# Performance work log

Hardware: AMD Instinct MI355X
Metric: run time of the kernel (lower is better)

Reference implementation:

```python
import jax, jax.numpy as jnp
import numpy as np

B, T, IN, H, L, OUT = 32, 512, 256, 1024, 2, 256


def setup_inputs() -> dict:
    key = jax.random.key(0)
    ks = jax.random.split(key, 12)
    s_in = 1.0 / np.sqrt(H)
    inp = {
        "input": jax.random.normal(ks[0], (B, T, IN), dtype=jnp.float32),
        # layer 0 GRU params (PyTorch layout: [3H, in], gate order r,z,n)
        "w_ih0": jax.random.uniform(ks[1], (3 * H, IN), jnp.float32, -s_in, s_in),
        "w_hh0": jax.random.uniform(ks[2], (3 * H, H), jnp.float32, -s_in, s_in),
        "b_ih0": jax.random.uniform(ks[3], (3 * H,), jnp.float32, -s_in, s_in),
        "b_hh0": jax.random.uniform(ks[4], (3 * H,), jnp.float32, -s_in, s_in),
        # layer 1 GRU params
        "w_ih1": jax.random.uniform(ks[5], (3 * H, H), jnp.float32, -s_in, s_in),
        "w_hh1": jax.random.uniform(ks[6], (3 * H, H), jnp.float32, -s_in, s_in),
        "b_ih1": jax.random.uniform(ks[7], (3 * H,), jnp.float32, -s_in, s_in),
        "b_hh1": jax.random.uniform(ks[8], (3 * H,), jnp.float32, -s_in, s_in),
        # final linear
        "fc_w": jax.random.uniform(ks[9], (OUT, H), jnp.float32, -s_in, s_in),
        "fc_b": jax.random.uniform(ks[10], (OUT,), jnp.float32, -s_in, s_in),
    }
    return inp


def _gru_layer(x, h0, w_ih, w_hh, b_ih, b_hh):
    # x: [B, T, D]; h0: [B, H]. Precompute all input projections at once.
    gx = jnp.einsum("btd,gd->btg", x, w_ih) + b_ih  # [B, T, 3H]

    def step(h, gx_t):
        gh = h @ w_hh.T + b_hh  # [B, 3H]
        xr, xz, xn = jnp.split(gx_t, 3, axis=-1)
        hr, hz, hn = jnp.split(gh, 3, axis=-1)
        r = jax.nn.sigmoid(xr + hr)
        z = jax.nn.sigmoid(xz + hz)
        n = jnp.tanh(xn + r * hn)
        h_new = (1.0 - z) * n + z * h
        return h_new, h_new

    h_last, hs = jax.lax.scan(step, h0, jnp.swapaxes(gx, 0, 1))  # hs: [T, B, H]
    return jnp.swapaxes(hs, 0, 1), h_last


def reference(input, w_ih0, w_hh0, b_ih0, b_hh0, w_ih1, w_hh1, b_ih1, b_hh1, fc_w, fc_b):
    b = input.shape[0]
    h0 = jnp.zeros((b, H), dtype=input.dtype)
    out0, h_last0 = _gru_layer(input, h0, w_ih0, w_hh0, b_ih0, b_hh0)
    out1, h_last1 = _gru_layer(out0, h0, w_ih1, w_hh1, b_ih1, b_hh1)
    h_n = jnp.stack([h_last0, h_last1], axis=0)  # [L, B, H]
    logits = out1[:, -1, :] @ fc_w.T + fc_b  # [B, OUT]
    return jax.nn.sigmoid(logits), h_n
```

## Files before the change

kernel.cpp:

```cpp
#include <hip/hip_runtime.h>

#define BB 32
#define TT 512
#define INW 256
#define HH 1024
#define OUTW 256
#define SLOT 32768

typedef __attribute__((ext_vector_type(8))) short short8;
typedef __attribute__((ext_vector_type(4))) float floatx4;

#define RSWZ(i) ((i) ^ ((((i) >> 5) & 3) << 2))

__device__ __forceinline__ unsigned short f2bf(float f) {
    unsigned int u = __float_as_uint(f);
    u = (u + 0x7fffu + ((u >> 16) & 1u)) >> 16;
    return (unsigned short)u;
}
__device__ __forceinline__ float bf2f(unsigned short h) {
    return __uint_as_float(((unsigned int)h) << 16);
}
__device__ __forceinline__ float fast_tanh(float x) {
    return 2.f / (1.f + __expf(-2.f * x)) - 1.f;
}

__global__ void cast_f32_bf16(const float* __restrict__ src,
                              unsigned short* __restrict__ dst, int n) {
    int i = blockIdx.x * blockDim.x + threadIdx.x;
    int stride = gridDim.x * blockDim.x;
    for (; i < n; i += stride) dst[i] = f2bf(src[i]);
}

template <int K>
__global__ __launch_bounds__(256) void gemm_gx(const unsigned short* __restrict__ X,
                                               const unsigned short* __restrict__ W,
                                               const float* __restrict__ bias,
                                               unsigned short* __restrict__ Cout) {
    __shared__ __align__(16) unsigned short As[64 * 40];
    __shared__ __align__(16) unsigned short Bs[64 * 40];
    int bid = blockIdx.x;
    int tn = bid % 48, tm = bid / 48;
    int tid = threadIdx.x;
    int lane = tid & 63, wv = tid >> 6;
    int wm = wv >> 1, wn = wv & 1;
    int l15 = lane & 15, q = lane >> 4;
    floatx4 acc[2][2] = {};
    int r = tid >> 2, kq = (tid & 3) * 8;
    const unsigned short* xrow = X + (size_t)(tm * 64 + r) * K;
    const unsigned short* wrow = W + (size_t)(tn * 64 + r) * K;
    const int NK = K / 32;
    for (int kk = 0; kk < NK; ++kk) {
        int k0 = kk * 32;
        *(short8*)&As[r * 40 + kq] = *(const short8*)&xrow[k0 + kq];
        *(short8*)&Bs[r * 40 + kq] = *(const short8*)&wrow[k0 + kq];
        __syncthreads();
        short8 a0 = *(const short8*)&As[(wm * 32 + l15) * 40 + q * 8];
        short8 a1 = *(const short8*)&As[(wm * 32 + 16 + l15) * 40 + q * 8];
        short8 b0 = *(const short8*)&Bs[(wn * 32 + l15) * 40 + q * 8];
        short8 b1 = *(const short8*)&Bs[(wn * 32 + 16 + l15) * 40 + q * 8];
        acc[0][0] = __builtin_amdgcn_mfma_f32_16x16x32_bf16(a0, b0, acc[0][0], 0, 0, 0);
        acc[0][1] = __builtin_amdgcn_mfma_f32_16x16x32_bf16(a0, b1, acc[0][1], 0, 0, 0);
        acc[1][0] = __builtin_amdgcn_mfma_f32_16x16x32_bf16(a1, b0, acc[1][0], 0, 0, 0);
        acc[1][1] = __builtin_amdgcn_mfma_f32_16x16x32_bf16(a1, b1, acc[1][1], 0, 0, 0);
        __syncthreads();
    }
    for (int mi = 0; mi < 2; ++mi)
        for (int ni = 0; ni < 2; ++ni) {
            int col = tn * 64 + wn * 32 + ni * 16 + l15;
            float bv = bias[col];
            int row0 = tm * 64 + wm * 32 + mi * 16 + q * 4;
            for (int rr = 0; rr < 4; ++rr) {
                Cout[(size_t)(row0 + rr) * 3072 + col] = f2bf(acc[mi][ni][rr] + bv);
            }
        }
}

__global__ __launch_bounds__(512, 2) void gru_fused(
    const unsigned short* __restrict__ gx0, const unsigned short* __restrict__ whh0,
    const float* __restrict__ bhh0, const unsigned short* __restrict__ wih1,
    const unsigned short* __restrict__ whh1, const float* __restrict__ bih1,
    const float* __restrict__ bhh1, unsigned short* __restrict__ ring0,
    unsigned short* __restrict__ ring1, float* __restrict__ hn0,
    float* __restrict__ hn1, unsigned int* __restrict__ flags) {
    __shared__ __align__(16) float red[8 * 6 * 64 * 4];
    const int bid = blockIdx.x;
    const int tid = threadIdx.x;
    const int lane = tid & 63, wv = tid >> 6;
    const int l15 = lane & 15, q = lane >> 4;
    const int gb = tid >> 3, gjh = tid & 7;
    const int gmi = gb >> 4, greg = gb & 3;
    const int grl = ((gb & 15) >> 2) * 16 + 2 * gjh;

    if (bid < 64) {
        const int j0 = bid * 16;
        const int kbase = wv * 128;
        const unsigned int* fl0 = flags + ((bid & 7) << 8);
        short8 Wr[4], Wz[4], Wn[4];
        {
            const unsigned short* wr0 = whh0 + (size_t)(j0 + l15) * HH;
            const unsigned short* wr1 = whh0 + (size_t)(1024 + j0 + l15) * HH;
            const unsigned short* wr2 = whh0 + (size_t)(2048 + j0 + l15) * HH;
#pragma unroll
            for (int s = 0; s < 4; ++s) {
                int k = kbase + s * 32 + q * 8;
                Wr[s] = *(const short8*)&wr0[k];
                Wz[s] = *(const short8*)&wr1[k];
                Wn[s] = *(const short8*)&wr2[k];
            }
        }
        float bR[2], bZ[2], bN[2], hpriv[2] = {0.f, 0.f};
        unsigned int pxr = 0, pxz = 0, pxn = 0;
        const unsigned short* gxp = nullptr;
        if (tid < 256) {
            int jj = j0 + 2 * gjh;
#pragma unroll
            for (int i = 0; i < 2; ++i) {
                bR[i] = bhh0[jj + i];
                bZ[i] = bhh0[1024 + jj + i];
                bN[i] = bhh0[2048 + jj + i];
            }
            gxp = gx0 + (size_t)gb * TT * 3072 + jj;
            pxr = *(const unsigned int*)(gxp);
            pxz = *(const unsigned int*)(gxp + 1024);
            pxn = *(const unsigned int*)(gxp + 2048);
        }

        for (int t = 0; t < TT; ++t) {
            if (t > 0 && wv == 0) {
                unsigned int target = (unsigned int)t;
                while (true) {
                    unsigned int v = __hip_atomic_load(fl0 + lane, __ATOMIC_RELAXED,
                                                       __HIP_MEMORY_SCOPE_AGENT);
                    if (__all((int)(v >= target))) break;
                    __builtin_amdgcn_s_sleep(1);
                }
            }
            __syncthreads();
            const unsigned short* hc = ring0 + (size_t)t * SLOT;
            unsigned int cxr = pxr, cxz = pxz, cxn = pxn;

            short8 A0[4], A1[4];
#pragma unroll
            for (int s = 0; s < 4; ++s) {
                int k = kbase + s * 32 + q * 8;
                int cb = (k >> 4) << 9, ko = k & 15;
                A0[s] = *(const short8*)&hc[cb + (l15 << 4) + ko];
                A1[s] = *(const short8*)&hc[cb + ((16 + l15) << 4) + ko];
            }
            floatx4 acc[6] = {};
#pragma unroll
            for (int s = 0; s < 4; ++s) {
                acc[0] = __builtin_amdgcn_mfma_f32_16x16x32_bf16(A0[s], Wr[s], acc[0], 0, 0, 0);
                acc[1] = __builtin_amdgcn_mfma_f32_16x16x32_bf16(A0[s], Wz[s], acc[1], 0, 0, 0);
                acc[2] = __builtin_amdgcn_mfma_f32_16x16x32_bf16(A0[s], Wn[s], acc[2], 0, 0, 0);
                acc[3] = __builtin_amdgcn_mfma_f32_16x16x32_bf16(A1[s], Wr[s], acc[3], 0, 0, 0);
                acc[4] = __builtin_amdgcn_mfma_f32_16x16x32_bf16(A1[s], Wz[s], acc[4], 0, 0, 0);
                acc[5] = __builtin_amdgcn_mfma_f32_16x16x32_bf16(A1[s], Wn[s], acc[5], 0, 0, 0);
            }
#pragma unroll
            for (int tl = 0; tl < 6; ++tl)
                *(floatx4*)&red[RSWZ(((wv * 6 + tl) * 64 + lane) * 4)] = acc[tl];
            __syncthreads();

            float hnew[2];
            if (tid < 256) {
#pragma unroll
                for (int i = 0; i < 2; ++i) {
                    int rl = grl + i;
                    float gr = 0.f, gz = 0.f, gn = 0.f;
#pragma unroll
                    for (int w = 0; w < 8; ++w) {
                        gr += red[RSWZ(((w * 6 + gmi * 3 + 0) * 64 + rl) * 4 + greg)];
                        gz += red[RSWZ(((w * 6 + gmi * 3 + 1) * 64 + rl) * 4 + greg)];
                        gn += red[RSWZ(((w * 6 + gmi * 3 + 2) * 64 + rl) * 4 + greg)];
                    }
                    float xr = bf2f((unsigned short)(i ? (cxr >> 16) : (cxr & 0xffffu)));
                    float xz = bf2f((unsigned short)(i ? (cxz >> 16) : (cxz & 0xffffu)));
                    float xn = bf2f((unsigned short)(i ? (cxn >> 16) : (cxn & 0xffffu)));
                    float rg = 1.f / (1.f + __expf(-(xr + gr + bR[i])));
                    float zg = 1.f / (1.f + __expf(-(xz + gz + bZ[i])));
                    float ng = fast_tanh(xn + rg * (gn + bN[i]));
                    hnew[i] = (1.f - zg) * ng + zg * hpriv[i];
                    hpriv[i] = hnew[i];
                }
                unsigned int hpack =
                    (unsigned int)f2bf(hnew[0]) | ((unsigned int)f2bf(hnew[1]) << 16);
                unsigned int* dst =
                    (unsigned int*)(ring0 + (size_t)(t + 1) * SLOT) + (bid << 8) + tid;
                __hip_atomic_store(dst, hpack, __ATOMIC_RELAXED,
                                   __HIP_MEMORY_SCOPE_AGENT);
                asm volatile("s_waitcnt vmcnt(0)" ::: "memory");
            }
            __syncthreads();
            if (tid < 8)
                __hip_atomic_store(flags + (tid << 8) + bid, (unsigned int)(t + 1),
                                   __ATOMIC_RELAXED, __HIP_MEMORY_SCOPE_AGENT);
            if (tid < 256) {
                if (t == TT - 1) {
                    hn0[gb * HH + j0 + 2 * gjh] = hnew[0];
                    hn0[gb * HH + j0 + 2 * gjh + 1] = hnew[1];
                }
                if (t + 1 < TT) {
                    const unsigned short* g2 = gxp + (size_t)(t + 1) * 3072;
                    pxr = *(const unsigned int*)(g2);
                    pxz = *(const unsigned int*)(g2 + 1024);
                    pxn = *(const unsigned int*)(g2 + 2048);
                }
            }
        }
    } else {
        const int b2 = bid - 64;
        const int j0 = b2 * 16;
        const bool isx = (wv >= 4);
        const int kbase = (wv & 3) * 256;
        const unsigned int* fl1 = flags + 2048 + ((b2 & 7) << 8);
        const unsigned int* fl0 = flags + ((b2 & 7) << 8);
        short8 Wr[8], Wz[8], Wn[8];
        {
            const unsigned short* wsrc = isx ? wih1 : whh1;
            const unsigned short* w0 = wsrc + (size_t)(j0 + l15) * HH;
            const unsigned short* w1 = wsrc + (size_t)(1024 + j0 + l15) * HH;
            const unsigned short* w2 = wsrc + (size_t)(2048 + j0 + l15) * HH;
#pragma unroll
            for (int s = 0; s < 8; ++s) {
                int k = kbase + s * 32 + q * 8;
                Wr[s] = *(const short8*)&w0[k];
                Wz[s] = *(const short8*)&w1[k];
                Wn[s] = *(const short8*)&w2[k];
            }
        }
        float cR[2], cZ[2], cNx[2], cNh[2], hpriv[2] = {0.f, 0.f};
        if (tid < 256) {
            int jj = j0 + 2 * gjh;
#pragma unroll
            for (int i = 0; i < 2; ++i) {
                cR[i] = bih1[jj + i] + bhh1[jj + i];
                cZ[i] = bih1[1024 + jj + i] + bhh1[1024 + jj + i];
                cNx[i] = bih1[2048 + jj + i];
                cNh[i] = bhh1[2048 + jj + i];
            }
        }

        for (int t = 0; t < TT; ++t) {
            if (t > 0 && wv == 0) {
                unsigned int target = (unsigned int)t;
                while (true) {
                    unsigned int v = __hip_atomic_load(fl1 + lane, __ATOMIC_RELAXED,
                                                       __HIP_MEMORY_SCOPE_AGENT);
                    if (__all((int)(v >= target))) break;
                    __builtin_amdgcn_s_sleep(1);
                }
            }
            if (wv == 4) {
                unsigned int target = (unsigned int)(t + 1);
                while (true) {
                    unsigned int v = __hip_atomic_load(fl0 + lane, __ATOMIC_RELAXED,
                                                       __HIP_MEMORY_SCOPE_AGENT);
                    if (__all((int)(v >= target))) break;
                    __builtin_amdgcn_s_sleep(1);
                }
            }
            __syncthreads();
            const unsigned short* src =
                isx ? (ring0 + (size_t)(t + 1) * SLOT) : (ring1 + (size_t)t * SLOT);

            short8 A0[8], A1[8];
#pragma unroll
            for (int s = 0; s < 8; ++s) {
                int k = kbase + s * 32 + q * 8;
                int cb = (k >> 4) << 9, ko = k & 15;
                A0[s] = *(const short8*)&src[cb + (l15 << 4) + ko];
                A1[s] = *(const short8*)&src[cb + ((16 + l15) << 4) + ko];
            }
            floatx4 acc[6] = {};
#pragma unroll
            for (int s = 0; s < 8; ++s) {
                acc[0] = __builtin_amdgcn_mfma_f32_16x16x32_bf16(A0[s], Wr[s], acc[0], 0, 0, 0);
                acc[1] = __builtin_amdgcn_mfma_f32_16x16x32_bf16(A0[s], Wz[s], acc[1], 0, 0, 0);
                acc[2] = __builtin_amdgcn_mfma_f32_16x16x32_bf16(A0[s], Wn[s], acc[2], 0, 0, 0);
                acc[3] = __builtin_amdgcn_mfma_f32_16x16x32_bf16(A1[s], Wr[s], acc[3], 0, 0, 0);
                acc[4] = __builtin_amdgcn_mfma_f32_16x16x32_bf16(A1[s], Wz[s], acc[4], 0, 0, 0);
                acc[5] = __builtin_amdgcn_mfma_f32_16x16x32_bf16(A1[s], Wn[s], acc[5], 0, 0, 0);
            }
#pragma unroll
            for (int tl = 0; tl < 6; ++tl)
                *(floatx4*)&red[RSWZ(((wv * 6 + tl) * 64 + lane) * 4)] = acc[tl];
            __syncthreads();

            float hnew[2];
            if (tid < 256) {
#pragma unroll
                for (int i = 0; i < 2; ++i) {
                    int rl = grl + i;
                    float gr = 0.f, gz = 0.f, hn = 0.f, xn = 0.f;
#pragma unroll
                    for (int w = 0; w < 4; ++w) {
                        gr += red[RSWZ(((w * 6 + gmi * 3 + 0) * 64 + rl) * 4 + greg)];
                        gz += red[RSWZ(((w * 6 + gmi * 3 + 1) * 64 + rl) * 4 + greg)];
                        hn += red[RSWZ(((w * 6 + gmi * 3 + 2) * 64 + rl) * 4 + greg)];
                    }
#pragma unroll
                    for (int w = 4; w < 8; ++w) {
                        gr += red[RSWZ(((w * 6 + gmi * 3 + 0) * 64 + rl) * 4 + greg)];
                        gz += red[RSWZ(((w * 6 + gmi * 3 + 1) * 64 + rl) * 4 + greg)];
                        xn += red[RSWZ(((w * 6 + gmi * 3 + 2) * 64 + rl) * 4 + greg)];
                    }
                    float rg = 1.f / (1.f + __expf(-(gr + cR[i])));
                    float zg = 1.f / (1.f + __expf(-(gz + cZ[i])));
                    float ng = fast_tanh(xn + cNx[i] + rg * (hn + cNh[i]));
                    hnew[i] = (1.f - zg) * ng + zg * hpriv[i];
                    hpriv[i] = hnew[i];
                }
                unsigned int hpack =
                    (unsigned int)f2bf(hnew[0]) | ((unsigned int)f2bf(hnew[1]) << 16);
                unsigned int* dst =
                    (unsigned int*)(ring1 + (size_t)(t + 1) * SLOT) + (b2 << 8) + tid;
                __hip_atomic_store(dst, hpack, __ATOMIC_RELAXED,
                                   __HIP_MEMORY_SCOPE_AGENT);
                asm volatile("s_waitcnt vmcnt(0)" ::: "memory");
            }
            __syncthreads();
            if (tid < 8)
                __hip_atomic_store(flags + 2048 + (tid << 8) + b2, (unsigned int)(t + 1),
                                   __ATOMIC_RELAXED, __HIP_MEMORY_SCOPE_AGENT);
            if (tid < 256 && t == TT - 1) {
                hn1[gb * HH + j0 + 2 * gjh] = hnew[0];
                hn1[gb * HH + j0 + 2 * gjh + 1] = hnew[1];
            }
        }
    }
}

__global__ void fc_out(const unsigned short* __restrict__ h1bf,
                       const float* __restrict__ fcw, const float* __restrict__ fcb,
                       float* __restrict__ out) {
    int b = blockIdx.x, o = threadIdx.x;
    const float* wr = fcw + (size_t)o * HH;
    float acc = fcb[o];
    for (int k = 0; k < HH; k += 16) {
        const unsigned short* hp = h1bf + ((k >> 4) << 9) + (b << 4);
#pragma unroll
        for (int i = 0; i < 16; ++i) acc += bf2f(hp[i]) * wr[k + i];
    }
    out[b * OUTW + o] = 1.f / (1.f + expf(-acc));
}

extern "C" void kernel_launch(void* const* d_in, const int* in_sizes, int n_in,
                              void* d_out, int out_size, void* d_ws, size_t ws_size,
                              hipStream_t stream) {
    (void)in_sizes; (void)n_in; (void)out_size; (void)ws_size;
    const float* input = (const float*)d_in[0];
    const float* w_ih0 = (const float*)d_in[1];
    const float* w_hh0 = (const float*)d_in[2];
    const float* b_ih0 = (const float*)d_in[3];
    const float* b_hh0 = (const float*)d_in[4];
    const float* w_ih1 = (const float*)d_in[5];
    const float* w_hh1 = (const float*)d_in[6];
    const float* b_ih1 = (const float*)d_in[7];
    const float* b_hh1 = (const float*)d_in[8];
    const float* fc_w = (const float*)d_in[9];
    const float* fc_b = (const float*)d_in[10];
    float* out = (float*)d_out;

    char* ws = (char*)d_ws;
    size_t off = 0;
    auto alloc = [&](size_t bytes) {
        void* p = ws + off;
        off += (bytes + 255) & ~(size_t)255;
        return p;
    };
    unsigned int* flags = (unsigned int*)alloc(16384);
    unsigned short* ring0 = (unsigned short*)alloc((size_t)(TT + 1) * SLOT * 2);
    unsigned short* ring1 = (unsigned short*)alloc((size_t)(TT + 1) * SLOT * 2);
    unsigned short* gx0 = (unsigned short*)alloc((size_t)16384 * 3072 * 2);
    unsigned short* in_bf = (unsigned short*)alloc((size_t)16384 * 256 * 2);
    unsigned short* wih0_bf = (unsigned short*)alloc((size_t)3072 * 256 * 2);
    unsigned short* whh0_bf = (unsigned short*)alloc((size_t)3072 * 1024 * 2);
    unsigned short* wih1_bf = (unsigned short*)alloc((size_t)3072 * 1024 * 2);
    unsigned short* whh1_bf = (unsigned short*)alloc((size_t)3072 * 1024 * 2);

    cast_f32_bf16<<<256, 256, 0, stream>>>(input, in_bf, 16384 * 256);
    cast_f32_bf16<<<64, 256, 0, stream>>>(w_ih0, wih0_bf, 3072 * 256);
    cast_f32_bf16<<<256, 256, 0, stream>>>(w_hh0, whh0_bf, 3072 * 1024);
    cast_f32_bf16<<<256, 256, 0, stream>>>(w_ih1, wih1_bf, 3072 * 1024);
    cast_f32_bf16<<<256, 256, 0, stream>>>(w_hh1, whh1_bf, 3072 * 1024);

    hipMemsetAsync(flags, 0, 16384, stream);
    hipMemsetAsync(ring0, 0, (size_t)SLOT * 2, stream);
    hipMemsetAsync(ring1, 0, (size_t)SLOT * 2, stream);

    gemm_gx<256><<<12288, 256, 0, stream>>>(in_bf, wih0_bf, b_ih0, gx0);

    gru_fused<<<128, 512, 0, stream>>>(gx0, whh0_bf, b_hh0, wih1_bf, whh1_bf, b_ih1,
                                       b_hh1, ring0, ring1, out + 8192,
                                       out + 8192 + 32768, flags);

    fc_out<<<32, 256, 0, stream>>>(ring1 + (size_t)TT * SLOT, fc_w, fc_b, out);
}
```

Before: 2.395 ms.

## Validate hidden-state ring data with sentinels instead of store-completion waits

The hidden-state ring buffers are pre-filled with a bf16 infinity sentinel pattern. Consumers now load h with cache-bypassing loads and re-poll until no sentinel remains, so producers no longer wait for their stores to complete before raising the step flag. The s_sleep calls in the flag spin loops are removed, and the cross-wave gate reductions become tree sums. This aims to shorten the per-step serial latency of the recurrence, at the cost of an extra ~67MB fill per call and busier spin-polling of global memory.

```diff
diff --git a/kernel.cpp b/kernel.cpp
--- a/kernel.cpp
+++ b/kernel.cpp
@@ -9,6 +9,9 @@
 
 typedef __attribute__((ext_vector_type(8))) short short8;
 typedef __attribute__((ext_vector_type(4))) float floatx4;
+typedef __attribute__((ext_vector_type(4))) unsigned int uint4v;
+
+#define SENT 0x7F807F80u
 
 #define RSWZ(i) ((i) ^ ((((i) >> 5) & 3) << 2))
 
@@ -22,6 +25,9 @@
 }
 __device__ __forceinline__ float fast_tanh(float x) {
     return 2.f / (1.f + __expf(-2.f * x)) - 1.f;
+}
+__device__ __forceinline__ float tree8(const float* p) {
+    return ((p[0] + p[1]) + (p[2] + p[3])) + ((p[4] + p[5]) + (p[6] + p[7]));
 }
 
 __global__ void cast_f32_bf16(const float* __restrict__ src,
@@ -29,6 +35,13 @@
     int i = blockIdx.x * blockDim.x + threadIdx.x;
     int stride = gridDim.x * blockDim.x;
     for (; i < n; i += stride) dst[i] = f2bf(src[i]);
+}
+
+__global__ void fill_sent(uint4v* __restrict__ dst, size_t n4) {
+    size_t i = (size_t)blockIdx.x * blockDim.x + threadIdx.x;
+    size_t stride = (size_t)gridDim.x * blockDim.x;
+    uint4v v = {SENT, SENT, SENT, SENT};
+    for (; i < n4; i += stride) dst[i] = v;
 }
 
 template <int K>
@@ -132,30 +145,53 @@
                     unsigned int v = __hip_atomic_load(fl0 + lane, __ATOMIC_RELAXED,
                                                        __HIP_MEMORY_SCOPE_AGENT);
                     if (__all((int)(v >= target))) break;
-                    __builtin_amdgcn_s_sleep(1);
                 }
             }
             __syncthreads();
             const unsigned short* hc = ring0 + (size_t)t * SLOT;
             unsigned int cxr = pxr, cxz = pxz, cxn = pxn;
 
-            short8 A0[4], A1[4];
+            const unsigned short* ap[4];
 #pragma unroll
             for (int s = 0; s < 4; ++s) {
                 int k = kbase + s * 32 + q * 8;
-                int cb = (k >> 4) << 9, ko = k & 15;
-                A0[s] = *(const short8*)&hc[cb + (l15 << 4) + ko];
-                A1[s] = *(const short8*)&hc[cb + ((16 + l15) << 4) + ko];
-            }
+                ap[s] = hc + ((k >> 4) << 9) + (l15 << 4) + (k & 15);
+            }
+            uint4v r0[4], r1[4];
+            while (true) {
+#pragma unroll
+                for (int s = 0; s < 4; ++s) {
+                    asm volatile("global_load_dwordx4 %0, %1, off sc0 sc1"
+                                 : "=&v"(r0[s]) : "v"(ap[s]));
+                    asm volatile("global_load_dwordx4 %0, %1, off offset:512 sc0 sc1"
+                                 : "=&v"(r1[s]) : "v"(ap[s]));
+                }
+                asm volatile("s_waitcnt vmcnt(0)"
+                             : "+v"(r0[0]), "+v"(r0[1]), "+v"(r0[2]), "+v"(r0[3]),
+                               "+v"(r1[0]), "+v"(r1[1]), "+v"(r1[2]), "+v"(r1[3])
+                             :: "memory");
+                unsigned bad = 0;
+#pragma unroll
+                for (int s = 0; s < 4; ++s) {
+                    bad |= (unsigned)(r0[s][0] == SENT) | (unsigned)(r0[s][1] == SENT) |
+                           (unsigned)(r0[s][2] == SENT) | (unsigned)(r0[s][3] == SENT);
+                    bad |= (unsigned)(r1[s][0] == SENT) | (unsigned)(r1[s][1] == SENT) |
+                           (unsigned)(r1[s][2] == SENT) | (unsigned)(r1[s][3] == SENT);
+                }
+                if (!__any((int)bad)) break;
+            }
+
             floatx4 acc[6] = {};
 #pragma unroll
             for (int s = 0; s < 4; ++s) {
-                acc[0] = __builtin_amdgcn_mfma_f32_16x16x32_bf16(A0[s], Wr[s], acc[0], 0, 0, 0);
-                acc[1] = __builtin_amdgcn_mfma_f32_16x16x32_bf16(A0[s], Wz[s], acc[1], 0, 0, 0);
-                acc[2] = __builtin_amdgcn_mfma_f32_16x16x32_bf16(A0[s], Wn[s], acc[2], 0, 0, 0);
-                acc[3] = __builtin_amdgcn_mfma_f32_16x16x32_bf16(A1[s], Wr[s], acc[3], 0, 0, 0);
-                acc[4] = __builtin_amdgcn_mfma_f32_16x16x32_bf16(A1[s], Wz[s], acc[4], 0, 0, 0);
-                acc[5] = __builtin_amdgcn_mfma_f32_16x16x32_bf16(A1[s], Wn[s], acc[5], 0, 0, 0);
+                short8 a0 = __builtin_bit_cast(short8, r0[s]);
+                short8 a1 = __builtin_bit_cast(short8, r1[s]);
+                acc[0] = __builtin_amdgcn_mfma_f32_16x16x32_bf16(a0, Wr[s], acc[0], 0, 0, 0);
+                acc[1] = __builtin_amdgcn_mfma_f32_16x16x32_bf16(a0, Wz[s], acc[1], 0, 0, 0);
+                acc[2] = __builtin_amdgcn_mfma_f32_16x16x32_bf16(a0, Wn[s], acc[2], 0, 0, 0);
+                acc[3] = __builtin_amdgcn_mfma_f32_16x16x32_bf16(a1, Wr[s], acc[3], 0, 0, 0);
+                acc[4] = __builtin_amdgcn_mfma_f32_16x16x32_bf16(a1, Wz[s], acc[4], 0, 0, 0);
+                acc[5] = __builtin_amdgcn_mfma_f32_16x16x32_bf16(a1, Wn[s], acc[5], 0, 0, 0);
             }
 #pragma unroll
             for (int tl = 0; tl < 6; ++tl)
@@ -167,13 +203,14 @@
 #pragma unroll
                 for (int i = 0; i < 2; ++i) {
                     int rl = grl + i;
-                    float gr = 0.f, gz = 0.f, gn = 0.f;
+                    float pr[8], pz[8], pn[8];
 #pragma unroll
                     for (int w = 0; w < 8; ++w) {
-                        gr += red[RSWZ(((w * 6 + gmi * 3 + 0) * 64 + rl) * 4 + greg)];
-                        gz += red[RSWZ(((w * 6 + gmi * 3 + 1) * 64 + rl) * 4 + greg)];
-                        gn += red[RSWZ(((w * 6 + gmi * 3 + 2) * 64 + rl) * 4 + greg)];
+                        pr[w] = red[RSWZ(((w * 6 + gmi * 3 + 0) * 64 + rl) * 4 + greg)];
+                        pz[w] = red[RSWZ(((w * 6 + gmi * 3 + 1) * 64 + rl) * 4 + greg)];
+                        pn[w] = red[RSWZ(((w * 6 + gmi * 3 + 2) * 64 + rl) * 4 + greg)];
                     }
+                    float gr = tree8(pr), gz = tree8(pz), gn = tree8(pn);
                     float xr = bf2f((unsigned short)(i ? (cxr >> 16) : (cxr & 0xffffu)));
                     float xz = bf2f((unsigned short)(i ? (cxz >> 16) : (cxz & 0xffffu)));
                     float xn = bf2f((unsigned short)(i ? (cxn >> 16) : (cxn & 0xffffu)));
@@ -189,7 +226,6 @@
                     (unsigned int*)(ring0 + (size_t)(t + 1) * SLOT) + (bid << 8) + tid;
                 __hip_atomic_store(dst, hpack, __ATOMIC_RELAXED,
                                    __HIP_MEMORY_SCOPE_AGENT);
-                asm volatile("s_waitcnt vmcnt(0)" ::: "memory");
             }
             __syncthreads();
             if (tid < 8)
@@ -248,7 +284,6 @@
                     unsigned int v = __hip_atomic_load(fl1 + lane, __ATOMIC_RELAXED,
                                                        __HIP_MEMORY_SCOPE_AGENT);
                     if (__all((int)(v >= target))) break;
-                    __builtin_amdgcn_s_sleep(1);
                 }
             }
             if (wv == 4) {
@@ -257,30 +292,55 @@
                     unsigned int v = __hip_atomic_load(fl0 + lane, __ATOMIC_RELAXED,
                                                        __HIP_MEMORY_SCOPE_AGENT);
                     if (__all((int)(v >= target))) break;
-                    __builtin_amdgcn_s_sleep(1);
                 }
             }
             __syncthreads();
             const unsigned short* src =
                 isx ? (ring0 + (size_t)(t + 1) * SLOT) : (ring1 + (size_t)t * SLOT);
 
-            short8 A0[8], A1[8];
+            const unsigned short* ap[8];
 #pragma unroll
             for (int s = 0; s < 8; ++s) {
                 int k = kbase + s * 32 + q * 8;
-                int cb = (k >> 4) << 9, ko = k & 15;
-                A0[s] = *(const short8*)&src[cb + (l15 << 4) + ko];
-                A1[s] = *(const short8*)&src[cb + ((16 + l15) << 4) + ko];
-            }
+                ap[s] = src + ((k >> 4) << 9) + (l15 << 4) + (k & 15);
+            }
+            uint4v r0[8], r1[8];
+            while (true) {
+#pragma unroll
+                for (int s = 0; s < 8; ++s) {
+                    asm volatile("global_load_dwordx4 %0, %1, off sc0 sc1"
+                                 : "=&v"(r0[s]) : "v"(ap[s]));
+                    asm volatile("global_load_dwordx4 %0, %1, off offset:512 sc0 sc1"
+                                 : "=&v"(r1[s]) : "v"(ap[s]));
+                }
+                asm volatile("s_waitcnt vmcnt(0)"
+                             : "+v"(r0[0]), "+v"(r0[1]), "+v"(r0[2]), "+v"(r0[3]),
+                               "+v"(r0[4]), "+v"(r0[5]), "+v"(r0[6]), "+v"(r0[7]),
+                               "+v"(r1[0]), "+v"(r1[1]), "+v"(r1[2]), "+v"(r1[3]),
+                               "+v"(r1[4]), "+v"(r1[5]), "+v"(r1[6]), "+v"(r1[7])
+                             :: "memory");
+                unsigned bad = 0;
+#pragma unroll
+                for (int s = 0; s < 8; ++s) {
+                    bad |= (unsigned)(r0[s][0] == SENT) | (unsigned)(r0[s][1] == SENT) |
+                           (unsigned)(r0[s][2] == SENT) | (unsigned)(r0[s][3] == SENT);
+                    bad |= (unsigned)(r1[s][0] == SENT) | (unsigned)(r1[s][1] == SENT) |
+                           (unsigned)(r1[s][2] == SENT) | (unsigned)(r1[s][3] == SENT);
+                }
+                if (!__any((int)bad)) break;
+            }
+
             floatx4 acc[6] = {};
 #pragma unroll
             for (int s = 0; s < 8; ++s) {
-                acc[0] = __builtin_amdgcn_mfma_f32_16x16x32_bf16(A0[s], Wr[s], acc[0], 0, 0, 0);
-                acc[1] = __builtin_amdgcn_mfma_f32_16x16x32_bf16(A0[s], Wz[s], acc[1], 0, 0, 0);
-                acc[2] = __builtin_amdgcn_mfma_f32_16x16x32_bf16(A0[s], Wn[s], acc[2], 0, 0, 0);
-                acc[3] = __builtin_amdgcn_mfma_f32_16x16x32_bf16(A1[s], Wr[s], acc[3], 0, 0, 0);
-                acc[4] = __builtin_amdgcn_mfma_f32_16x16x32_bf16(A1[s], Wz[s], acc[4], 0, 0, 0);
-                acc[5] = __builtin_amdgcn_mfma_f32_16x16x32_bf16(A1[s], Wn[s], acc[5], 0, 0, 0);
+                short8 a0 = __builtin_bit_cast(short8, r0[s]);
+                short8 a1 = __builtin_bit_cast(short8, r1[s]);
+                acc[0] = __builtin_amdgcn_mfma_f32_16x16x32_bf16(a0, Wr[s], acc[0], 0, 0, 0);
+                acc[1] = __builtin_amdgcn_mfma_f32_16x16x32_bf16(a0, Wz[s], acc[1], 0, 0, 0);
+                acc[2] = __builtin_amdgcn_mfma_f32_16x16x32_bf16(a0, Wn[s], acc[2], 0, 0, 0);
+                acc[3] = __builtin_amdgcn_mfma_f32_16x16x32_bf16(a1, Wr[s], acc[3], 0, 0, 0);
+                acc[4] = __builtin_amdgcn_mfma_f32_16x16x32_bf16(a1, Wz[s], acc[4], 0, 0, 0);
+                acc[5] = __builtin_amdgcn_mfma_f32_16x16x32_bf16(a1, Wn[s], acc[5], 0, 0, 0);
             }
 #pragma unroll
             for (int tl = 0; tl < 6; ++tl)
@@ -292,19 +352,21 @@
 #pragma unroll
                 for (int i = 0; i < 2; ++i) {
                     int rl = grl + i;
-                    float gr = 0.f, gz = 0.f, hn = 0.f, xn = 0.f;
-#pragma unroll
-                    for (int w = 0; w < 4; ++w) {
-                        gr += red[RSWZ(((w * 6 + gmi * 3 + 0) * 64 + rl) * 4 + greg)];
-                        gz += red[RSWZ(((w * 6 + gmi * 3 + 1) * 64 + rl) * 4 + greg)];
-                        hn += red[RSWZ(((w * 6 + gmi * 3 + 2) * 64 + rl) * 4 + greg)];
+                    float pr[8], pz[8], ph[4], px[4];
+#pragma unroll
+                    for (int w = 0; w < 8; ++w) {
+                        pr[w] = red[RSWZ(((w * 6 + gmi * 3 + 0) * 64 + rl) * 4 + greg)];
+                        pz[w] = red[RSWZ(((w * 6 + gmi * 3 + 1) * 64 + rl) * 4 + greg)];
                     }
 #pragma unroll
-                    for (int w = 4; w < 8; ++w) {
-                        gr += red[RSWZ(((w * 6 + gmi * 3 + 0) * 64 + rl) * 4 + greg)];
-                        gz += red[RSWZ(((w * 6 + gmi * 3 + 1) * 64 + rl) * 4 + greg)];
-                        xn += red[RSWZ(((w * 6 + gmi * 3 + 2) * 64 + rl) * 4 + greg)];
-                    }
+                    for (int w = 0; w < 4; ++w)
+                        ph[w] = red[RSWZ(((w * 6 + gmi * 3 + 2) * 64 + rl) * 4 + greg)];
+#pragma unroll
+                    for (int w = 4; w < 8; ++w)
+                        px[w - 4] = red[RSWZ(((w * 6 + gmi * 3 + 2) * 64 + rl) * 4 + greg)];
+                    float gr = tree8(pr), gz = tree8(pz);
+                    float hn = (ph[0] + ph[1]) + (ph[2] + ph[3]);
+                    float xn = (px[0] + px[1]) + (px[2] + px[3]);
                     float rg = 1.f / (1.f + __expf(-(gr + cR[i])));
                     float zg = 1.f / (1.f + __expf(-(gz + cZ[i])));
                     float ng = fast_tanh(xn + cNx[i] + rg * (hn + cNh[i]));
@@ -317,7 +379,6 @@
                     (unsigned int*)(ring1 + (size_t)(t + 1) * SLOT) + (b2 << 8) + tid;
                 __hip_atomic_store(dst, hpack, __ATOMIC_RELAXED,
                                    __HIP_MEMORY_SCOPE_AGENT);
-                asm volatile("s_waitcnt vmcnt(0)" ::: "memory");
             }
             __syncthreads();
             if (tid < 8)
@@ -379,6 +440,11 @@
     unsigned short* wih1_bf = (unsigned short*)alloc((size_t)3072 * 1024 * 2);
     unsigned short* whh1_bf = (unsigned short*)alloc((size_t)3072 * 1024 * 2);
 
+    {
+        size_t total_bytes = (size_t)2 * (TT + 1) * SLOT * 2;
+        fill_sent<<<1024, 256, 0, stream>>>((uint4v*)ring0, total_bytes / 16);
+    }
+
     cast_f32_bf16<<<256, 256, 0, stream>>>(input, in_bf, 16384 * 256);
     cast_f32_bf16<<<64, 256, 0, stream>>>(w_ih0, wih0_bf, 3072 * 256);
     cast_f32_bf16<<<256, 256, 0, stream>>>(w_hh0, whh0_bf, 3072 * 1024);
```

New measurement: 2.455 ms. +2.5%, slower.
